# Kernel tuning notes

Measured on AMD Instinct MI355X. Metric: run time of the kernel, lower is better.

The kernel has to match this reference:

```python
import jax, jax.numpy as jnp
import numpy as np
from jax import lax

K_EDGE = 4096  # fixed padded size for per-(b,c) edge point sets


def _min_pool2d_3x3(x):
    # torch: -max_pool2d(-x, 3, 1, 1); maxpool pads with -inf, so minpool pads with +inf
    return lax.reduce_window(x, jnp.inf, lax.min,
                             (1, 1, 3, 3), (1, 1, 1, 1),
                             [(0, 0), (0, 0), (1, 1), (1, 1)])


def _get_edges(mask):
    ero = _min_pool2d_3x3(mask)
    return jnp.logical_xor(ero > 0.5, mask > 0.5)  # [B,C,H,W] bool


def _ahd_loss_one(gedge, pedge, coords):
    # gedge, pedge: [N] bool flattened edge masks; coords: [N,2] float32 pixel coords
    n_g = gedge.sum().astype(jnp.float32)
    n_p = pedge.sum().astype(jnp.float32)
    ar = jnp.arange(K_EDGE)
    gidx = jnp.nonzero(gedge, size=K_EDGE, fill_value=0)[0]
    pidx = jnp.nonzero(pedge, size=K_EDGE, fill_value=0)[0]
    gvalid = ar < n_g
    pvalid = ar < n_p
    gc = coords[gidx]  # [K,2]
    pc = coords[pidx]  # [K,2]
    # pairwise Euclidean distances [K,K]
    d = jnp.sqrt(((gc[:, None, :] - pc[None, :, :]) ** 2).sum(-1))
    # for each gth edge point: distance to nearest pred edge point (== EDT of pred edges)
    dg = jnp.min(jnp.where(pvalid[None, :], d, jnp.inf), axis=1)
    gth2pred = jnp.where(gvalid, dg, 0.0).sum() / n_g
    # for each pred edge point: distance to nearest gth edge point
    dp = jnp.min(jnp.where(gvalid[:, None], d, jnp.inf), axis=0)
    pred2gth = jnp.where(pvalid, dp, 0.0).sum() / n_p
    ahd = (gth2pred + pred2gth) / 2.0
    ahd = jnp.where((n_g == 0) & (n_p == 0), jnp.nan, ahd)
    return 1.0 - 1.0 / (1.0 + ahd)


def setup_inputs() -> dict:
    key = jax.random.key(0)
    B, C, H, W = 8, 2, 256, 256
    k1, k2 = jax.random.split(key)
    # smooth blob-like soft masks: low-res noise upsampled -> realistic contours
    gth = jax.image.resize(jax.random.uniform(k1, (B, C, 12, 12), jnp.float32),
                           (B, C, H, W), method='bilinear')
    pred = jax.image.resize(jax.random.uniform(k2, (B, C, 12, 12), jnp.float32),
                            (B, C, H, W), method='bilinear')
    return {"gth": gth, "pred": pred}


def reference(gth, pred):
    B, C, H, W = gth.shape
    gth_b = (gth > 0.5).astype(jnp.float32)
    pred_b = (pred > 0.5).astype(jnp.float32)
    gedges = _get_edges(gth_b).reshape(B * C, H * W)
    pedges = _get_edges(pred_b).reshape(B * C, H * W)
    yy, xx = jnp.meshgrid(jnp.arange(H), jnp.arange(W), indexing='ij')
    coords = jnp.stack([yy, xx], axis=-1).reshape(H * W, 2).astype(jnp.float32)
    losses = jax.vmap(_ahd_loss_one, in_axes=(0, 0, None))(gedges, pedges, coords)
    return jnp.nanmean(losses)
```

## Files before the change

### kernel.cpp

```cpp
#include <hip/hip_runtime.h>
#include <math.h>

#define HH 256
#define WW 256
#define HWSZ (HH * WW)
#define KE 4096
#define NSLICE 16
#define NCH 64
#define GSENT 1024

typedef unsigned long long u64;
typedef unsigned short u16;

__global__ void __launch_bounds__(256) binarize_pack(
        const float* __restrict__ gth, const float* __restrict__ pred,
        u64* __restrict__ bm) {
    int b = blockIdx.x;
    int tensor = b >> 12;
    int sr = b & 4095;
    const float* img = tensor ? pred : gth;
    float v = img[sr * WW + threadIdx.x];
    u64 bal = __ballot(v > 0.5f);
    int lane = threadIdx.x & 63;
    int wave = threadIdx.x >> 6;
    if (lane == 0) bm[(size_t)b * 4 + wave] = bal;
}

__global__ void __launch_bounds__(256) edge_edt(
        const u64* __restrict__ bm,
        float2* __restrict__ gpts, float2* __restrict__ ppts,
        int* __restrict__ gcnt, int* __restrict__ pcnt,
        u16* __restrict__ G16) {
    int b = blockIdx.x;
    int tensor = b >> 4;
    int slice = b & 15;
    const u64* rm = bm + (size_t)(tensor * 4096 + slice * 256) * 4;
    float2* pts = (tensor ? ppts : gpts) + slice * KE;
    int* cnt = (tensor ? pcnt : gcnt) + slice;

    __shared__ int sc[256];
    __shared__ u64 ebl[1024];

    int row = threadIdx.x;
    u64 vc[4], va[4], vb[4];
#pragma unroll
    for (int w = 0; w < 4; ++w) {
        vc[w] = rm[row * 4 + w];
        va[w] = (row > 0) ? rm[(row - 1) * 4 + w] : ~0ull;
        vb[w] = (row < HH - 1) ? rm[(row + 1) * 4 + w] : ~0ull;
    }
    u64 vert[4];
#pragma unroll
    for (int w = 0; w < 4; ++w) vert[w] = va[w] & vc[w] & vb[w];
    u64 e[4];
#pragma unroll
    for (int w = 0; w < 4; ++w) {
        u64 left  = (vert[w] << 1) | ((w > 0) ? (vert[w - 1] >> 63) : 1ull);
        u64 right = (vert[w] >> 1) | (((w < 3) ? (vert[w + 1] & 1ull) : 1ull) << 63);
        e[w] = vc[w] & ~(vert[w] & left & right);
    }
    int mycnt = __popcll(e[0]) + __popcll(e[1]) + __popcll(e[2]) + __popcll(e[3]);

    sc[row] = mycnt;
    __syncthreads();
    for (int d = 1; d < 256; d <<= 1) {
        int v = (row >= d) ? sc[row - d] : 0;
        __syncthreads();
        sc[row] += v;
        __syncthreads();
    }
    int off = sc[row] - mycnt;

    int rem = KE - off;
    u64 t[4];
    if (rem >= mycnt) {
#pragma unroll
        for (int w = 0; w < 4; ++w) t[w] = e[w];
    } else if (rem <= 0) {
#pragma unroll
        for (int w = 0; w < 4; ++w) t[w] = 0ull;
    } else {
        int k = rem;
#pragma unroll
        for (int w = 0; w < 4; ++w) {
            int pc = __popcll(e[w]);
            if (k >= pc) { t[w] = e[w]; k -= pc; }
            else {
                u64 bits = e[w], keep = 0ull;
                for (int i = 0; i < k; ++i) {
                    u64 low = bits & (~bits + 1ull);
                    keep |= low;
                    bits ^= low;
                }
                t[w] = keep;
                k = 0;
            }
        }
    }
#pragma unroll
    for (int w = 0; w < 4; ++w) ebl[row * 4 + w] = t[w];

    int o = off;
#pragma unroll
    for (int w = 0; w < 4; ++w) {
        u64 bits = e[w];
        while (bits) {
            int l = __ffsll((long long)bits) - 1;
            bits &= bits - 1;
            if (o < KE) pts[o] = make_float2((float)row, (float)(w * 64 + l));
            ++o;
        }
    }
    if (row == HH - 1) *cnt = sc[HH - 1];
    __syncthreads();

    int c = threadIdx.x;
    int cw = c >> 6, cb = c & 63;
    u16* G = G16 + (size_t)b * HWSZ;
    int g = GSENT;
    for (int r = 0; r < HH; ++r) {
        int bit = (int)((ebl[r * 4 + cw] >> cb) & 1ull);
        g = bit ? 0 : min(g + 1, GSENT);
        G[r * WW + c] = (u16)g;
    }
    __syncthreads();
    int gu = GSENT;
    for (int r = HH - 1; r >= 0; --r) {
        int bit = (int)((ebl[r * 4 + cw] >> cb) & 1ull);
        gu = bit ? 0 : min(gu + 1, GSENT);
        int gf = min((int)G[r * WW + c], gu);
        G[r * WW + c] = (u16)gf;
    }
}

__global__ void __launch_bounds__(64) nn_gather(
        const float2* __restrict__ gpts, const float2* __restrict__ ppts,
        const int* __restrict__ gcnt, const int* __restrict__ pcnt,
        const u16* __restrict__ G16, float* __restrict__ partial) {
    int b = blockIdx.x;
    int chunk = b & (NCH - 1);
    int sd = b >> 6;
    int dir = sd & 1;
    int slice = sd >> 1;
    int tid = threadIdx.x;

    int qfull = dir ? pcnt[slice] : gcnt[slice];
    int qc = min(qfull, KE);
    int qi = chunk * 64 + tid;

    float val = 0.0f;
    if (qi < qc) {
        const float2* q = (dir ? ppts : gpts) + slice * KE;
        int tt = dir ? 0 : 1;
        const u16* G = G16 + (size_t)(tt * 16 + slice) * HWSZ;
        float2 qp = q[qi];
        int r = (int)qp.x, c = (int)qp.y;
        const int4* grow = (const int4*)(G + r * WW);
        int m = 0x7fffffff;
#pragma unroll
        for (int j = 0; j < 32; ++j) {
            int4 v = grow[j];
            int base = j * 8;
#define STEP(word, k0)                                                      \
            {                                                               \
                int g0 = (word) & 0xffff;                                   \
                int g1 = (int)(((unsigned)(word)) >> 16);                   \
                int dc0 = c - (base + k0);                                  \
                int dc1 = c - (base + k0 + 1);                              \
                m = min(m, dc0 * dc0 + g0 * g0);                            \
                m = min(m, dc1 * dc1 + g1 * g1);                            \
            }
            STEP(v.x, 0) STEP(v.y, 2) STEP(v.z, 4) STEP(v.w, 6)
#undef STEP
        }
        val = sqrtf((float)m);
    }
    for (int s = 32; s > 0; s >>= 1) val += __shfl_xor(val, s, 64);
    if (tid == 0) partial[b] = val;
}

__global__ void __launch_bounds__(512) finalize3(
        const int* __restrict__ gcnt, const int* __restrict__ pcnt,
        const float* __restrict__ partial, float* __restrict__ out) {
    int tid = threadIdx.x;
    float v = partial[tid * 4] + partial[tid * 4 + 1] +
              partial[tid * 4 + 2] + partial[tid * 4 + 3];
    v += __shfl_xor(v, 1, 16);
    v += __shfl_xor(v, 2, 16);
    v += __shfl_xor(v, 4, 16);
    v += __shfl_xor(v, 8, 16);
    __shared__ float sdsum[32];
    if ((tid & 15) == 0) sdsum[tid >> 4] = v;
    __syncthreads();
    if (tid == 0) {
        float sum = 0.0f;
        int nvalid = 0;
        for (int s = 0; s < NSLICE; ++s) {
            int ng = gcnt[s];
            int np_ = pcnt[s];
            if (ng > 0 && np_ > 0) {
                float ahd = 0.5f * (sdsum[s * 2 + 0] / (float)ng +
                                    sdsum[s * 2 + 1] / (float)np_);
                sum += 1.0f - 1.0f / (1.0f + ahd);
                nvalid++;
            }
        }
        out[0] = nvalid ? (sum / (float)nvalid) : NAN;
    }
}

extern "C" void kernel_launch(void* const* d_in, const int* in_sizes, int n_in,
                              void* d_out, int out_size, void* d_ws, size_t ws_size,
                              hipStream_t stream) {
    const float* gth = (const float*)d_in[0];
    const float* pred = (const float*)d_in[1];
    float* out = (float*)d_out;
    char* ws = (char*)d_ws;

    u64* bm = (u64*)(ws);
    float2* gpts = (float2*)(ws + 262144);
    float2* ppts = (float2*)(ws + 786432);
    u16* G16 = (u16*)(ws + 1310720);
    int* gcnt = (int*)(ws + 5505024);
    int* pcnt = (int*)(ws + 5505088);
    float* partial = (float*)(ws + 5505152);

    binarize_pack<<<8192, 256, 0, stream>>>(gth, pred, bm);
    edge_edt<<<32, 256, 0, stream>>>(bm, gpts, ppts, gcnt, pcnt, G16);
    nn_gather<<<NSLICE * 2 * NCH, 64, 0, stream>>>(gpts, ppts, gcnt, pcnt, G16, partial);
    finalize3<<<1, 512, 0, stream>>>(gcnt, pcnt, partial, out);
}
```

Baseline: 47.26 us.

## Split vertical EDT into separate kernel parallelized over row blocks

The edge extraction and compaction kernel no longer computes the per-column vertical distance map. It writes the edge bitmask to workspace, and a new 256-block kernel builds that map instead. Each thread transposes its column into four 64-bit words and finds the nearest edge row with bit-scan operations over 32-row chunks. Before, each of only 32 blocks ran two serial 256-step sweeps with a global read-modify-write. The cost is an extra kernel launch, an extra bitmask round trip through global memory, and a redundant column transpose in each of the eight blocks that share a map.

```diff
diff --git a/kernel.cpp b/kernel.cpp
--- a/kernel.cpp
+++ b/kernel.cpp
@@ -8,6 +8,7 @@
 #define NSLICE 16
 #define NCH 64
 #define GSENT 1024
+#define RPB 32
 
 typedef unsigned long long u64;
 typedef unsigned short u16;
@@ -26,20 +27,18 @@
     if (lane == 0) bm[(size_t)b * 4 + wave] = bal;
 }
 
-__global__ void __launch_bounds__(256) edge_edt(
+__global__ void __launch_bounds__(256) edge_compact(
         const u64* __restrict__ bm,
         float2* __restrict__ gpts, float2* __restrict__ ppts,
-        int* __restrict__ gcnt, int* __restrict__ pcnt,
-        u16* __restrict__ G16) {
+        u64* __restrict__ ebm,
+        int* __restrict__ gcnt, int* __restrict__ pcnt) {
     int b = blockIdx.x;
     int tensor = b >> 4;
     int slice = b & 15;
     const u64* rm = bm + (size_t)(tensor * 4096 + slice * 256) * 4;
     float2* pts = (tensor ? ppts : gpts) + slice * KE;
     int* cnt = (tensor ? pcnt : gcnt) + slice;
-
-    __shared__ int sc[256];
-    __shared__ u64 ebl[1024];
+    u64* eb = ebm + (size_t)b * 1024;
 
     int row = threadIdx.x;
     u64 vc[4], va[4], vb[4];
@@ -61,6 +60,7 @@
     }
     int mycnt = __popcll(e[0]) + __popcll(e[1]) + __popcll(e[2]) + __popcll(e[3]);
 
+    __shared__ int sc[256];
     sc[row] = mycnt;
     __syncthreads();
     for (int d = 1; d < 256; d <<= 1) {
@@ -98,7 +98,7 @@
         }
     }
 #pragma unroll
-    for (int w = 0; w < 4; ++w) ebl[row * 4 + w] = t[w];
+    for (int w = 0; w < 4; ++w) eb[row * 4 + w] = t[w];
 
     int o = off;
 #pragma unroll
@@ -112,24 +112,52 @@
         }
     }
     if (row == HH - 1) *cnt = sc[HH - 1];
+}
+
+__device__ __forceinline__ int word_dist(u64 w, int p) {
+    if (w == 0) return GSENT;
+    int lo = __ffsll((long long)w) - 1;
+    int hi = 63 - __clzll((long long)w);
+    if (p <= lo) return lo - p;
+    if (p >= hi) return p - hi;
+    u64 up = w >> p;
+    int du = __ffsll((long long)up) - 1;
+    u64 dn = w << (63 - p);
+    int dd = __clzll((long long)dn);
+    return min(du, dd);
+}
+
+__global__ void __launch_bounds__(256) edt_vert(
+        const u64* __restrict__ ebm, u16* __restrict__ G16) {
+    int map = blockIdx.x >> 3;
+    int rblk = blockIdx.x & 7;
+    const u64* eb = ebm + (size_t)map * 1024;
+    u16* G = G16 + (size_t)map * HWSZ;
+
+    __shared__ u64 ebl[1024];
+    int tid = threadIdx.x;
+    for (int i = tid; i < 1024; i += 256) ebl[i] = eb[i];
     __syncthreads();
 
-    int c = threadIdx.x;
-    int cw = c >> 6, cb = c & 63;
-    u16* G = G16 + (size_t)b * HWSZ;
-    int g = GSENT;
-    for (int r = 0; r < HH; ++r) {
-        int bit = (int)((ebl[r * 4 + cw] >> cb) & 1ull);
-        g = bit ? 0 : min(g + 1, GSENT);
-        G[r * WW + c] = (u16)g;
-    }
-    __syncthreads();
-    int gu = GSENT;
-    for (int r = HH - 1; r >= 0; --r) {
-        int bit = (int)((ebl[r * 4 + cw] >> cb) & 1ull);
-        gu = bit ? 0 : min(gu + 1, GSENT);
-        int gf = min((int)G[r * WW + c], gu);
-        G[r * WW + c] = (u16)gf;
+    int c = tid, cw = c >> 6, cb = c & 63;
+    u64 w0 = 0, w1 = 0, w2 = 0, w3 = 0;
+#pragma unroll 4
+    for (int r = 0; r < 64; ++r) {
+        w0 |= ((ebl[(r      ) * 4 + cw] >> cb) & 1ull) << r;
+        w1 |= ((ebl[(r +  64) * 4 + cw] >> cb) & 1ull) << r;
+        w2 |= ((ebl[(r + 128) * 4 + cw] >> cb) & 1ull) << r;
+        w3 |= ((ebl[(r + 192) * 4 + cw] >> cb) & 1ull) << r;
+    }
+
+    int r0 = rblk * RPB;
+#pragma unroll 4
+    for (int i = 0; i < RPB; ++i) {
+        int r = r0 + i;
+        int d = word_dist(w0, r);
+        d = min(d, word_dist(w1, r - 64));
+        d = min(d, word_dist(w2, r - 128));
+        d = min(d, word_dist(w3, r - 192));
+        G[r * WW + c] = (u16)min(d, GSENT);
     }
 }
 
@@ -218,15 +246,17 @@
     char* ws = (char*)d_ws;
 
     u64* bm = (u64*)(ws);
-    float2* gpts = (float2*)(ws + 262144);
-    float2* ppts = (float2*)(ws + 786432);
-    u16* G16 = (u16*)(ws + 1310720);
-    int* gcnt = (int*)(ws + 5505024);
-    int* pcnt = (int*)(ws + 5505088);
-    float* partial = (float*)(ws + 5505152);
+    u64* ebm = (u64*)(ws + 262144);
+    float2* gpts = (float2*)(ws + 524288);
+    float2* ppts = (float2*)(ws + 1048576);
+    u16* G16 = (u16*)(ws + 1572864);
+    int* gcnt = (int*)(ws + 5767168);
+    int* pcnt = (int*)(ws + 5767232);
+    float* partial = (float*)(ws + 5767296);
 
     binarize_pack<<<8192, 256, 0, stream>>>(gth, pred, bm);
-    edge_edt<<<32, 256, 0, stream>>>(bm, gpts, ppts, gcnt, pcnt, G16);
+    edge_compact<<<32, 256, 0, stream>>>(bm, gpts, ppts, ebm, gcnt, pcnt);
+    edt_vert<<<256, 256, 0, stream>>>(ebm, G16);
     nn_gather<<<NSLICE * 2 * NCH, 64, 0, stream>>>(gpts, ppts, gcnt, pcnt, G16, partial);
     finalize3<<<1, 512, 0, stream>>>(gcnt, pcnt, partial, out);
 }
```

Measured after the change: 46.74 us. About the same (-1.1%).

## Fuse column EDT and NN gather into shared-memory kernel with last-block finalize

Applied to the files above, without the earlier changes.

Moves the per-column vertical distance transform out of the serial edge kernel into the NN kernel. Each 1024-thread block rebuilds the full 256x256 u16 distance grid in LDS, split into four row bands with a boundary fix-up, and stores it with an XOR swizzle. Gathers then read LDS instead of a global grid. The finalize kernel is replaced by an atomic-counter last-block reduction, and the block prefix scan uses wave shuffles. The cost is that each of the 8 splits per slice/direction recomputes the same grid, and the kernel needs a 147 KB dynamic LDS allocation.

```diff
diff --git a/kernel.cpp b/kernel.cpp
--- a/kernel.cpp
+++ b/kernel.cpp
@@ -3,43 +3,41 @@
 
 #define HH 256
 #define WW 256
-#define HWSZ (HH * WW)
 #define KE 4096
 #define NSLICE 16
-#define NCH 64
-#define GSENT 1024
+#define NSPLIT 8
+#define QPB (KE / NSPLIT)
+#define NBLK (NSLICE * 2 * NSPLIT)
+#define GCAP 1024
 
 typedef unsigned long long u64;
 typedef unsigned short u16;
 
-__global__ void __launch_bounds__(256) binarize_pack(
+__global__ void __launch_bounds__(256) k1_binpack(
         const float* __restrict__ gth, const float* __restrict__ pred,
-        u64* __restrict__ bm) {
+        u64* __restrict__ bm, int* __restrict__ counter) {
     int b = blockIdx.x;
+    if (b == 0 && threadIdx.x == 0) *counter = 0;
     int tensor = b >> 12;
     int sr = b & 4095;
     const float* img = tensor ? pred : gth;
     float v = img[sr * WW + threadIdx.x];
     u64 bal = __ballot(v > 0.5f);
-    int lane = threadIdx.x & 63;
-    int wave = threadIdx.x >> 6;
-    if (lane == 0) bm[(size_t)b * 4 + wave] = bal;
-}
-
-__global__ void __launch_bounds__(256) edge_edt(
+    if ((threadIdx.x & 63) == 0) bm[(size_t)b * 4 + (threadIdx.x >> 6)] = bal;
+}
+
+__global__ void __launch_bounds__(256) k2_edge_compact(
         const u64* __restrict__ bm,
         float2* __restrict__ gpts, float2* __restrict__ ppts,
-        int* __restrict__ gcnt, int* __restrict__ pcnt,
-        u16* __restrict__ G16) {
+        u64* __restrict__ ebm,
+        int* __restrict__ gcnt, int* __restrict__ pcnt) {
     int b = blockIdx.x;
     int tensor = b >> 4;
     int slice = b & 15;
     const u64* rm = bm + (size_t)(tensor * 4096 + slice * 256) * 4;
     float2* pts = (tensor ? ppts : gpts) + slice * KE;
     int* cnt = (tensor ? pcnt : gcnt) + slice;
-
-    __shared__ int sc[256];
-    __shared__ u64 ebl[1024];
+    u64* eb = ebm + (size_t)b * 1024;
 
     int row = threadIdx.x;
     u64 vc[4], va[4], vb[4];
@@ -61,15 +59,18 @@
     }
     int mycnt = __popcll(e[0]) + __popcll(e[1]) + __popcll(e[2]) + __popcll(e[3]);
 
-    sc[row] = mycnt;
-    __syncthreads();
-    for (int d = 1; d < 256; d <<= 1) {
-        int v = (row >= d) ? sc[row - d] : 0;
-        __syncthreads();
-        sc[row] += v;
-        __syncthreads();
-    }
-    int off = sc[row] - mycnt;
+    int lane = row & 63, wv = row >> 6;
+    int incl = mycnt;
+    for (int d = 1; d < 64; d <<= 1) {
+        int n = __shfl_up(incl, d, 64);
+        if (lane >= d) incl += n;
+    }
+    __shared__ int wsum[4];
+    if (lane == 63) wsum[wv] = incl;
+    __syncthreads();
+    int wpre = 0;
+    for (int k = 0; k < 4; ++k) wpre += (k < wv) ? wsum[k] : 0;
+    int off = wpre + incl - mycnt;
 
     int rem = KE - off;
     u64 t[4];
@@ -98,7 +99,7 @@
         }
     }
 #pragma unroll
-    for (int w = 0; w < 4; ++w) ebl[row * 4 + w] = t[w];
+    for (int w = 0; w < 4; ++w) eb[row * 4 + w] = t[w];
 
     int o = off;
 #pragma unroll
@@ -111,64 +112,94 @@
             ++o;
         }
     }
-    if (row == HH - 1) *cnt = sc[HH - 1];
-    __syncthreads();
-
-    int c = threadIdx.x;
-    int cw = c >> 6, cb = c & 63;
-    u16* G = G16 + (size_t)b * HWSZ;
-    int g = GSENT;
-    for (int r = 0; r < HH; ++r) {
-        int bit = (int)((ebl[r * 4 + cw] >> cb) & 1ull);
-        g = bit ? 0 : min(g + 1, GSENT);
-        G[r * WW + c] = (u16)g;
-    }
-    __syncthreads();
-    int gu = GSENT;
-    for (int r = HH - 1; r >= 0; --r) {
-        int bit = (int)((ebl[r * 4 + cw] >> cb) & 1ull);
-        gu = bit ? 0 : min(gu + 1, GSENT);
-        int gf = min((int)G[r * WW + c], gu);
-        G[r * WW + c] = (u16)gf;
-    }
-}
-
-__global__ void __launch_bounds__(64) nn_gather(
+    if (row == HH - 1) *cnt = wpre + incl;
+}
+
+__device__ __forceinline__ int gidx(int r, int c) {
+    int cj = (c >> 3) ^ (r & 7);
+    return r * WW + cj * 8 + (c & 7);
+}
+
+__global__ void __launch_bounds__(1024) k3_sd_nn(
         const float2* __restrict__ gpts, const float2* __restrict__ ppts,
         const int* __restrict__ gcnt, const int* __restrict__ pcnt,
-        const u16* __restrict__ G16, float* __restrict__ partial) {
-    int b = blockIdx.x;
-    int chunk = b & (NCH - 1);
-    int sd = b >> 6;
+        const u64* __restrict__ ebm,
+        float* __restrict__ partial, int* __restrict__ counter,
+        float* __restrict__ out) {
+    extern __shared__ char smem[];
+    u64* ebl  = (u64*)smem;
+    int* slo  = (int*)(smem + 8192);
+    int* shi  = (int*)(smem + 12288);
+    u16* G    = (u16*)(smem + 16384);
+    float* red = (float*)(smem + 8192);
+    __shared__ int s_last;
+
+    int bid = blockIdx.x;
+    int split = bid & (NSPLIT - 1);
+    int sd = bid >> 3;
     int dir = sd & 1;
     int slice = sd >> 1;
     int tid = threadIdx.x;
 
+    int tt = dir ? 0 : 1;
+    const u64* eb = ebm + (size_t)(tt * 16 + slice) * 1024;
+    ebl[tid] = eb[tid];
+    __syncthreads();
+
+    int c = tid & 255, rb = tid >> 8, base = rb << 6;
+    int cw = c >> 6, cb = c & 63;
+    u64 w = 0;
+#pragma unroll 8
+    for (int i = 0; i < 64; ++i)
+        w |= ((ebl[(base + i) * 4 + cw] >> cb) & 1ull) << i;
+    slo[c * 4 + rb] = w ? base + (__ffsll((long long)w) - 1) : 100000;
+    shi[c * 4 + rb] = w ? base + (63 - __clzll((long long)w)) : -100000;
+    __syncthreads();
+    int hiA = -100000, loB = 100000;
+#pragma unroll
+    for (int k = 0; k < 4; ++k) {
+        int lok = slo[c * 4 + k], hik = shi[c * 4 + k];
+        if (k < rb) hiA = max(hiA, hik);
+        if (k > rb) loB = min(loB, lok);
+    }
+    int g = min(base - 1 - hiA, GCAP);
+    for (int i = 0; i < 64; ++i) {
+        int bit = (int)((w >> i) & 1ull);
+        g = bit ? 0 : min(g + 1, GCAP);
+        G[gidx(base + i, c)] = (u16)g;
+    }
+    int gu = min(loB - (base + 64), GCAP);
+    for (int i = 63; i >= 0; --i) {
+        int bit = (int)((w >> i) & 1ull);
+        gu = bit ? 0 : min(gu + 1, GCAP);
+        int ix = gidx(base + i, c);
+        G[ix] = (u16)min((int)G[ix], gu);
+    }
+    __syncthreads();
+
     int qfull = dir ? pcnt[slice] : gcnt[slice];
     int qc = min(qfull, KE);
-    int qi = chunk * 64 + tid;
-
     float val = 0.0f;
-    if (qi < qc) {
+    int qi = split * QPB + tid;
+    if (tid < QPB && qi < qc) {
         const float2* q = (dir ? ppts : gpts) + slice * KE;
-        int tt = dir ? 0 : 1;
-        const u16* G = G16 + (size_t)(tt * 16 + slice) * HWSZ;
         float2 qp = q[qi];
-        int r = (int)qp.x, c = (int)qp.y;
-        const int4* grow = (const int4*)(G + r * WW);
+        int r = (int)qp.x, cc = (int)qp.y;
+        const uint4* grow = (const uint4*)(G + r * WW);
+        int rsw = r & 7;
         int m = 0x7fffffff;
 #pragma unroll
         for (int j = 0; j < 32; ++j) {
-            int4 v = grow[j];
-            int base = j * 8;
+            uint4 v = grow[j ^ rsw];
+            int bs = j * 8;
 #define STEP(word, k0)                                                      \
             {                                                               \
-                int g0 = (word) & 0xffff;                                   \
-                int g1 = (int)(((unsigned)(word)) >> 16);                   \
-                int dc0 = c - (base + k0);                                  \
-                int dc1 = c - (base + k0 + 1);                              \
-                m = min(m, dc0 * dc0 + g0 * g0);                            \
-                m = min(m, dc1 * dc1 + g1 * g1);                            \
+                int g0 = (int)((word) & 0xffffu);                           \
+                int g1 = (int)((word) >> 16);                               \
+                int d0 = cc - (bs + k0);                                    \
+                int d1 = cc - (bs + k0 + 1);                                \
+                m = min(m, d0 * d0 + g0 * g0);                              \
+                m = min(m, d1 * d1 + g1 * g1);                              \
             }
             STEP(v.x, 0) STEP(v.y, 2) STEP(v.z, 4) STEP(v.w, 6)
 #undef STEP
@@ -176,36 +207,43 @@
         val = sqrtf((float)m);
     }
     for (int s = 32; s > 0; s >>= 1) val += __shfl_xor(val, s, 64);
-    if (tid == 0) partial[b] = val;
-}
-
-__global__ void __launch_bounds__(512) finalize3(
-        const int* __restrict__ gcnt, const int* __restrict__ pcnt,
-        const float* __restrict__ partial, float* __restrict__ out) {
-    int tid = threadIdx.x;
-    float v = partial[tid * 4] + partial[tid * 4 + 1] +
-              partial[tid * 4 + 2] + partial[tid * 4 + 3];
-    v += __shfl_xor(v, 1, 16);
-    v += __shfl_xor(v, 2, 16);
-    v += __shfl_xor(v, 4, 16);
-    v += __shfl_xor(v, 8, 16);
-    __shared__ float sdsum[32];
-    if ((tid & 15) == 0) sdsum[tid >> 4] = v;
-    __syncthreads();
+    if ((tid & 63) == 0) red[tid >> 6] = val;
+    __syncthreads();
+
     if (tid == 0) {
-        float sum = 0.0f;
-        int nvalid = 0;
-        for (int s = 0; s < NSLICE; ++s) {
-            int ng = gcnt[s];
-            int np_ = pcnt[s];
-            if (ng > 0 && np_ > 0) {
-                float ahd = 0.5f * (sdsum[s * 2 + 0] / (float)ng +
-                                    sdsum[s * 2 + 1] / (float)np_);
-                sum += 1.0f - 1.0f / (1.0f + ahd);
-                nvalid++;
+        float qsum = 0.0f;
+        for (int k = 0; k < 16; ++k) qsum += red[k];
+        __hip_atomic_store(&partial[bid], qsum, __ATOMIC_RELEASE,
+                           __HIP_MEMORY_SCOPE_AGENT);
+        int prev = __hip_atomic_fetch_add(counter, 1, __ATOMIC_ACQ_REL,
+                                          __HIP_MEMORY_SCOPE_AGENT);
+        s_last = (prev == NBLK - 1) ? 1 : 0;
+    }
+    __syncthreads();
+    if (s_last) {
+        if (tid < NBLK)
+            red[tid] = __hip_atomic_load(&partial[tid], __ATOMIC_RELAXED,
+                                         __HIP_MEMORY_SCOPE_AGENT);
+        __syncthreads();
+        if (tid == 0) {
+            float sum = 0.0f;
+            int nvalid = 0;
+            for (int s = 0; s < NSLICE; ++s) {
+                int ng = gcnt[s];
+                int np_ = pcnt[s];
+                if (ng > 0 && np_ > 0) {
+                    float gs = 0.0f, ps = 0.0f;
+                    for (int k = 0; k < NSPLIT; ++k) {
+                        gs += red[(s * 2 + 0) * NSPLIT + k];
+                        ps += red[(s * 2 + 1) * NSPLIT + k];
+                    }
+                    float ahd = 0.5f * (gs / (float)ng + ps / (float)np_);
+                    sum += 1.0f - 1.0f / (1.0f + ahd);
+                    nvalid++;
+                }
             }
-        }
-        out[0] = nvalid ? (sum / (float)nvalid) : NAN;
+            out[0] = nvalid ? (sum / (float)nvalid) : NAN;
+        }
     }
 }
 
@@ -218,15 +256,16 @@
     char* ws = (char*)d_ws;
 
     u64* bm = (u64*)(ws);
-    float2* gpts = (float2*)(ws + 262144);
-    float2* ppts = (float2*)(ws + 786432);
-    u16* G16 = (u16*)(ws + 1310720);
-    int* gcnt = (int*)(ws + 5505024);
-    int* pcnt = (int*)(ws + 5505088);
-    float* partial = (float*)(ws + 5505152);
-
-    binarize_pack<<<8192, 256, 0, stream>>>(gth, pred, bm);
-    edge_edt<<<32, 256, 0, stream>>>(bm, gpts, ppts, gcnt, pcnt, G16);
-    nn_gather<<<NSLICE * 2 * NCH, 64, 0, stream>>>(gpts, ppts, gcnt, pcnt, G16, partial);
-    finalize3<<<1, 512, 0, stream>>>(gcnt, pcnt, partial, out);
-}
+    u64* ebm = (u64*)(ws + 262144);
+    float2* gpts = (float2*)(ws + 524288);
+    float2* ppts = (float2*)(ws + 1048576);
+    int* gcnt = (int*)(ws + 1572864);
+    int* pcnt = (int*)(ws + 1572928);
+    float* partial = (float*)(ws + 1572992);
+    int* counter = (int*)(ws + 1574016);
+
+    k1_binpack<<<8192, 256, 0, stream>>>(gth, pred, bm, counter);
+    k2_edge_compact<<<32, 256, 0, stream>>>(bm, gpts, ppts, ebm, gcnt, pcnt);
+    k3_sd_nn<<<NBLK, 1024, 147456, stream>>>(gpts, ppts, gcnt, pcnt, ebm,
+                                             partial, counter, out);
+}
```

New measurement: 76.61 us. 62.1% more time.
